# Kernel tuning notes

Hardware: AMD Instinct MI355X
Metric: run time of the kernel (lower is better)

The kernel has to match this reference:

```python
import jax, jax.numpy as jnp
import numpy as np

NUM_HEADS = 16
THETA = 10000.0
B, S, D = 2, 2048, 1024
D_K = D // NUM_HEADS


def setup_inputs() -> dict:
    key = jax.random.key(0)
    ks = jax.random.split(key, 5)
    s = 0.02
    return {
        "x": jax.random.normal(ks[0], (B, S, D), dtype=jnp.float32),
        "W_q": jax.random.normal(ks[1], (D, D), dtype=jnp.float32) * s,
        "W_k": jax.random.normal(ks[2], (D, D), dtype=jnp.float32) * s,
        "W_v": jax.random.normal(ks[3], (D, D), dtype=jnp.float32) * s,
        "W_o": jax.random.normal(ks[4], (D, D), dtype=jnp.float32) * s,
        "token_positions": jnp.arange(S, dtype=jnp.int32),
    }


def _rope(x, token_positions):
    # x: [..., seq, d_k]; equivalent to the block-diagonal 2x2 rotation matmul
    d2 = x.shape[-1] // 2
    inv_freq = THETA ** (-(2.0 * jnp.arange(d2, dtype=x.dtype)) / x.shape[-1])  # [d2]
    ang = token_positions.astype(x.dtype)[:, None] * inv_freq[None, :]  # [seq, d2]
    cos, sin = jnp.cos(ang), jnp.sin(ang)
    xp = x.reshape(x.shape[:-1] + (d2, 2))
    xe, xo = xp[..., 0], xp[..., 1]
    oe = cos * xe - sin * xo
    oo = sin * xe + cos * xo
    return jnp.stack([oe, oo], axis=-1).reshape(x.shape)


def reference(x, W_q, W_k, W_v, W_o, token_positions):
    seq = x.shape[-2]
    # QKV projections (weights stored as [out, in])
    Q = jnp.einsum('bsd,ed->bse', x, W_q)
    K = jnp.einsum('bsd,ed->bse', x, W_k)
    V = jnp.einsum('bsd,ed->bse', x, W_v)
    def split_heads(t):
        return t.reshape(t.shape[:-1] + (NUM_HEADS, D_K)).swapaxes(-3, -2)  # [b,h,s,dk]
    Q, K, V = split_heads(Q), split_heads(K), split_heads(V)
    Q = _rope(Q, token_positions)
    K = _rope(K, token_positions)
    scale = 1.0 / np.sqrt(D_K)
    scores = jnp.einsum('bhqd,bhkd->bhqk', Q, K) * scale
    causal = jnp.tril(jnp.ones((seq, seq), dtype=bool))
    scores = jnp.where(causal, scores, -jnp.inf)
    probs = jax.nn.softmax(scores, axis=-1)
    out = jnp.einsum('bhqk,bhkd->bhqd', probs, V)
    out = out.swapaxes(-3, -2).reshape(x.shape[:-1] + (D,))
    return jnp.einsum('bse,de->bsd', out, W_o)
```

## Files before the change

### kernel.cpp

```cpp
#include <hip/hip_runtime.h>
#include <hip/hip_bf16.h>
#include <math.h>

#define H_    16
#define DK_   64
#define Dm    1024
#define Bb    2
#define Ss    2048
#define Mrows 4096
#define QSCALE 0.1803368801f

typedef short s16x8 __attribute__((ext_vector_type(8)));
typedef float f32x4 __attribute__((ext_vector_type(4)));
typedef unsigned short u16;
typedef unsigned int u32;

__device__ __forceinline__ u16 f2b(float f) {
  __hip_bfloat16 h = __float2bfloat16(f);
  return *reinterpret_cast<u16*>(&h);
}
__device__ __forceinline__ float b2f(u16 u) {
  __hip_bfloat16 h;
  *reinterpret_cast<u16*>(&h) = u;
  return __bfloat162float(h);
}
__device__ __forceinline__ u32 pkbf(float hi, float lo) {
  return __builtin_amdgcn_perm(__float_as_uint(hi), __float_as_uint(lo), 0x07060302u);
}

#define GLDS(g, l)                                                             \
  __builtin_amdgcn_global_load_lds(                                            \
      (const __attribute__((address_space(1))) unsigned int*)(g),              \
      (__attribute__((address_space(3))) unsigned int*)(l), 16, 0, 0)

__device__ __forceinline__ int SW64(int row, int col) {
  return row * 64 + ((((col >> 3) ^ (row & 7) ^ (row >> 3)) & 7) << 3) + (col & 7);
}

__global__ __launch_bounds__(256) void k_castall(
    const float* __restrict__ x,  const float* __restrict__ Wq,
    const float* __restrict__ Wk, const float* __restrict__ Wv,
    const float* __restrict__ Wo,
    u16* __restrict__ xb,  u16* __restrict__ wqb, u16* __restrict__ wkb,
    u16* __restrict__ wvb, u16* __restrict__ wob,
    const int* __restrict__ pos, float2* __restrict__ tab) {
  if (blockIdx.x >= 8192) {
    int t = (blockIdx.x - 8192) * 256 + threadIdx.x;
    int s = t >> 5, i = t & 31;
    float p = (float)pos[s];
    float ang = p * powf(10000.0f, -(float)i / 32.0f);
    tab[t] = make_float2(cosf(ang), sinf(ang));
    return;
  }
  int i = blockIdx.x * 256 + threadIdx.x;
  const float* s;
  u16* d;
  int off;
  if (i < 1048576) { s = x; d = xb; off = i; }
  else {
    int j = i - 1048576;
    int w = j >> 18;
    off = j & 262143;
    s = (w == 0) ? Wq : (w == 1) ? Wk : (w == 2) ? Wv : Wo;
    d = (w == 0) ? wqb : (w == 1) ? wkb : (w == 2) ? wvb : wob;
  }
  float4 v = reinterpret_cast<const float4*>(s)[off];
  ushort4 o;
  o.x = f2b(v.x); o.y = f2b(v.y); o.z = f2b(v.z); o.w = f2b(v.w);
  reinterpret_cast<ushort4*>(d)[off] = o;
}

__global__ __launch_bounds__(256) void k_ropeK(u16* __restrict__ K,
                                               const float2* __restrict__ tab) {
  int t = blockIdx.x * 256 + threadIdx.x;
  int row = t >> 7;
  int c0 = (t & 127) << 3;
  int i0 = (c0 & 63) >> 1;
  const float2* tb = &tab[(row & (Ss - 1)) * 32 + i0];
  float2 cs[4];
#pragma unroll
  for (int j = 0; j < 4; ++j) cs[j] = tb[j];
  size_t off = (size_t)row * Dm + c0;
  s16x8 k = *reinterpret_cast<const s16x8*>(&K[off]);
  s16x8 ko;
#pragma unroll
  for (int j = 0; j < 4; ++j) {
    float ke = b2f((u16)k[2 * j]), kd = b2f((u16)k[2 * j + 1]);
    ko[2 * j]     = (short)f2b(cs[j].x * ke - cs[j].y * kd);
    ko[2 * j + 1] = (short)f2b(cs[j].y * ke + cs[j].x * kd);
  }
  *reinterpret_cast<s16x8*>(&K[off]) = ko;
}

template <int BN, bool QKV>
__global__ __launch_bounds__(256) void k_gemm(
    const u16* __restrict__ A, const u16* __restrict__ B,
    u16* __restrict__ OQ, u16* __restrict__ OK2, u16* __restrict__ OVT,
    float* __restrict__ OF, int K) {
  constexpr int NFR = BN / 32;
  __shared__ __align__(16) u16 lsA[2][128 * 32];
  __shared__ __align__(16) u16 lsB[2][BN * 32];
  const int tid = threadIdx.x, lane = tid & 63, wave = tid >> 6;
  const int quad = lane >> 4, l16 = lane & 15;
  const int wrow = wave >> 1, wcol = wave & 1;
  const int n0 = blockIdx.x * BN, m0 = blockIdx.y * 128;
  f32x4 acc[4][NFR] = {};

  auto stage = [&](int k0, int bi) {
#pragma unroll
    for (int c = 0; c < 2; ++c) {
      int f = (wave * 2 + c) * 64 + lane;
      int row = f >> 2;
      int gs = (f & 3) ^ ((row >> 1) & 3);
      GLDS(A + (size_t)(m0 + row) * K + k0 + gs * 8, &lsA[bi][(wave * 2 + c) * 512]);
    }
#pragma unroll
    for (int c = 0; c < NFR / 2; ++c) {
      int f = (wave * (NFR / 2) + c) * 64 + lane;
      int row = f >> 2;
      int gs = (f & 3) ^ ((row >> 1) & 3);
      GLDS(B + (size_t)(n0 + row) * K + k0 + gs * 8, &lsB[bi][(wave * (NFR / 2) + c) * 512]);
    }
  };

  stage(0, 0);
  int bi = 0;
  for (int k0 = 0; k0 < K; k0 += 32) {
    __syncthreads();
    if (k0 + 32 < K) stage(k0 + 32, bi ^ 1);
    s16x8 af[4], bfr[NFR];
#pragma unroll
    for (int i = 0; i < 4; ++i) {
      int row = wrow * 64 + i * 16 + l16;
      af[i] = *reinterpret_cast<const s16x8*>(
          &lsA[bi][row * 32 + ((quad ^ ((row >> 1) & 3)) << 3)]);
    }
#pragma unroll
    for (int i = 0; i < NFR; ++i) {
      int row = wcol * (BN / 2) + i * 16 + l16;
      bfr[i] = *reinterpret_cast<const s16x8*>(
          &lsB[bi][row * 32 + ((quad ^ ((row >> 1) & 3)) << 3)]);
    }
#pragma unroll
    for (int mi = 0; mi < 4; ++mi)
#pragma unroll
      for (int ni = 0; ni < NFR; ++ni)
        acc[mi][ni] = __builtin_amdgcn_mfma_f32_16x16x32_bf16(af[mi], bfr[ni], acc[mi][ni], 0, 0, 0);
    bi ^= 1;
  }

  if (QKV) {
    const int which = n0 >> 10;
    const int nbase = (n0 & 1023) + wcol * (BN / 2);
    if (which == 2) {
#pragma unroll
      for (int mi = 0; mi < 4; ++mi)
#pragma unroll
        for (int ni = 0; ni < NFR; ++ni) {
          int row0 = m0 + wrow * 64 + mi * 16 + quad * 4;
          int col  = nbase + ni * 16 + l16;
          int bb = row0 >> 11, s0 = row0 & (Ss - 1);
          ushort4 pk;
          pk.x = f2b(acc[mi][ni][0]); pk.y = f2b(acc[mi][ni][1]);
          pk.z = f2b(acc[mi][ni][2]); pk.w = f2b(acc[mi][ni][3]);
          *reinterpret_cast<ushort4*>(&OVT[((size_t)bb * Dm + col) * Ss + s0]) = pk;
        }
    } else {
      u16* Op = which ? OK2 : OQ;
#pragma unroll
      for (int mi = 0; mi < 4; ++mi)
#pragma unroll
        for (int ni = 0; ni < NFR; ++ni)
#pragma unroll
          for (int r = 0; r < 4; ++r) {
            int row = m0 + wrow * 64 + mi * 16 + quad * 4 + r;
            int col = nbase + ni * 16 + l16;
            Op[(size_t)row * Dm + col] = f2b(acc[mi][ni][r]);
          }
    }
  } else {
#pragma unroll
    for (int mi = 0; mi < 4; ++mi)
#pragma unroll
      for (int ni = 0; ni < NFR; ++ni)
#pragma unroll
        for (int r = 0; r < 4; ++r) {
          int row = m0 + wrow * 64 + mi * 16 + quad * 4 + r;
          int col = n0 + wcol * (BN / 2) + ni * 16 + l16;
          OF[(size_t)row * Dm + col] = acc[mi][ni][r];
        }
  }
}

__global__ __launch_bounds__(256) void k_flash(const u16* __restrict__ Q,
                                               const u16* __restrict__ K,
                                               const u16* __restrict__ VT,
                                               u16* __restrict__ O,
                                               const float2* __restrict__ tab) {
  __shared__ __align__(16) u16 lsK[4][64 * 64];
  __shared__ __align__(16) u16 lsVT[4][64 * 64];
  __shared__ __align__(16) u16 lsP[4][32 * 64];
  const int tid = threadIdx.x, lane = tid & 63, wave = tid >> 6;
  const int quad = lane >> 4, l16 = lane & 15;
  const int bid = blockIdx.x;
  const int bh = bid & 31;
  const int h = bh & (H_ - 1), b = bh >> 4;
  const int g = bid >> 5, a = g & 7, bsel = g >> 3;
  const int qt = bsel ? (15 - a) : a;
  const int q0 = qt * 128;
  const int qbase = q0 + wave * 32;
  const int ktmax_w = (qbase + 31) >> 6;
  const int xorv = (l16 * 2) & 0xE;

  s16x8 qf[2][2];
#pragma unroll
  for (int s = 0; s < 2; ++s) {
    const int qpos = qbase + s * 16 + l16;
    const size_t qoff = (size_t)(b * Ss + qpos) * Dm + h * 64;
    s16x8 r0 = *reinterpret_cast<const s16x8*>(&Q[qoff + quad * 8]);
    s16x8 r1 = *reinterpret_cast<const s16x8*>(&Q[qoff + 32 + quad * 8]);
    const float2* tb = &tab[(qpos & (Ss - 1)) * 32];
#pragma unroll
    for (int kc = 0; kc < 2; ++kc) {
      s16x8 raw = kc ? r1 : r0;
#pragma unroll
      for (int p = 0; p < 4; ++p) {
        float2 cs = tb[kc * 16 + quad * 4 + p];
        float e = b2f((u16)raw[2 * p]), o = b2f((u16)raw[2 * p + 1]);
        qf[s][kc][2 * p]     = (short)f2b((cs.x * e - cs.y * o) * QSCALE);
        qf[s][kc][2 * p + 1] = (short)f2b((cs.y * e + cs.x * o) * QSCALE);
      }
    }
  }
  s16x8 ones;
#pragma unroll
  for (int j = 0; j < 8; ++j) ones[j] = (short)0x3F80;

  f32x4 ot[2][4] = {};
  f32x4 lAcc[2] = {};

  auto stagepair = [&](int pp) {
#pragma unroll
    for (int half = 0; half < 2; ++half) {
      const int kt = pp * 2 + half;
      const int slot = kt & 3;
      const size_t kbase  = (size_t)(b * Ss + kt * 64) * Dm + h * 64;
      const size_t vtbase = ((size_t)b * Dm + h * 64) * Ss + kt * 64;
#pragma unroll
      for (int c = 0; c < 2; ++c) {
        int sl = (wave * 2 + c) * 64 + lane;
        int row = sl >> 3;
        int gg = ((sl & 7) ^ (row & 7) ^ (row >> 3)) & 7;
        GLDS(K  + kbase  + (size_t)row * Dm + gg * 8, &lsK[slot][(wave * 2 + c) * 512]);
        GLDS(VT + vtbase + (size_t)row * Ss + gg * 8, &lsVT[slot][(wave * 2 + c) * 512]);
      }
    }
  };

  stagepair(0);
  for (int pp = 0; pp <= qt; ++pp) {
    __syncthreads();
    if (pp < qt) stagepair(pp + 1);
    const int kt0 = 2 * pp;

    f32x4 st[2][2][4] = {};
#pragma unroll
    for (int half = 0; half < 2; ++half) {
      const int kt = kt0 + half;
      if (kt > ktmax_w) break;
      const int slot = kt & 3;
#pragma unroll
      for (int kc = 0; kc < 2; ++kc)
#pragma unroll
        for (int ni = 0; ni < 4; ++ni) {
          s16x8 kf = *reinterpret_cast<const s16x8*>(
              &lsK[slot][SW64(ni * 16 + l16, kc * 32 + quad * 8)]);
          st[half][0][ni] = __builtin_amdgcn_mfma_f32_16x16x32_bf16(kf, qf[0][kc], st[half][0][ni], 0, 0, 0);
          st[half][1][ni] = __builtin_amdgcn_mfma_f32_16x16x32_bf16(kf, qf[1][kc], st[half][1][ni], 0, 0, 0);
        }
    }
#pragma unroll
    for (int half = 0; half < 2; ++half) {
      const int kt = kt0 + half;
      if (kt > ktmax_w) break;
      const int slot = kt & 3;
      if (kt == ktmax_w) {
#pragma unroll
        for (int s = 0; s < 2; ++s) {
          int gq = qbase + s * 16 + l16;
#pragma unroll
          for (int ni = 0; ni < 4; ++ni)
#pragma unroll
            for (int r = 0; r < 4; ++r)
              if (kt * 64 + ni * 16 + quad * 4 + r > gq) st[half][s][ni][r] = -INFINITY;
        }
      }
#pragma unroll
      for (int s = 0; s < 2; ++s)
#pragma unroll
        for (int ni = 0; ni < 4; ++ni) {
          float e0 = __builtin_amdgcn_exp2f(st[half][s][ni][0]);
          float e1 = __builtin_amdgcn_exp2f(st[half][s][ni][1]);
          float e2 = __builtin_amdgcn_exp2f(st[half][s][ni][2]);
          float e3 = __builtin_amdgcn_exp2f(st[half][s][ni][3]);
          uint2 pk;
          pk.x = pkbf(e1, e0);
          pk.y = pkbf(e3, e2);
          *reinterpret_cast<uint2*>(
              &lsP[wave][(s * 16 + l16) * 64 + (((ni * 4 + quad) ^ xorv) << 2)]) = pk;
        }
#pragma unroll
      for (int kc = 0; kc < 2; ++kc) {
        s16x8 pf0 = *reinterpret_cast<const s16x8*>(
            &lsP[wave][l16 * 64 + (((kc * 8 + quad * 2) ^ xorv) << 2)]);
        s16x8 pf1 = *reinterpret_cast<const s16x8*>(
            &lsP[wave][(16 + l16) * 64 + (((kc * 8 + quad * 2) ^ xorv) << 2)]);
        lAcc[0] = __builtin_amdgcn_mfma_f32_16x16x32_bf16(ones, pf0, lAcc[0], 0, 0, 0);
        lAcc[1] = __builtin_amdgcn_mfma_f32_16x16x32_bf16(ones, pf1, lAcc[1], 0, 0, 0);
#pragma unroll
        for (int ni = 0; ni < 4; ++ni) {
          s16x8 vf = *reinterpret_cast<const s16x8*>(
              &lsVT[slot][SW64(ni * 16 + l16, kc * 32 + quad * 8)]);
          ot[0][ni] = __builtin_amdgcn_mfma_f32_16x16x32_bf16(vf, pf0, ot[0][ni], 0, 0, 0);
          ot[1][ni] = __builtin_amdgcn_mfma_f32_16x16x32_bf16(vf, pf1, ot[1][ni], 0, 0, 0);
        }
      }
    }
  }

#pragma unroll
  for (int s = 0; s < 2; ++s) {
    float inv = 1.0f / lAcc[s][0];
    const size_t obase = (size_t)(b * Ss + qbase + s * 16 + l16) * Dm + h * 64;
#pragma unroll
    for (int ni = 0; ni < 4; ++ni) {
      ushort4 pk;
      pk.x = f2b(ot[s][ni][0] * inv); pk.y = f2b(ot[s][ni][1] * inv);
      pk.z = f2b(ot[s][ni][2] * inv); pk.w = f2b(ot[s][ni][3] * inv);
      *reinterpret_cast<ushort4*>(&O[obase + ni * 16 + quad * 4]) = pk;
    }
  }
}

extern "C" void kernel_launch(void* const* d_in, const int* in_sizes, int n_in,
                              void* d_out, int out_size, void* d_ws, size_t ws_size,
                              hipStream_t stream) {
  const float* x  = (const float*)d_in[0];
  const float* Wq = (const float*)d_in[1];
  const float* Wk = (const float*)d_in[2];
  const float* Wv = (const float*)d_in[3];
  const float* Wo = (const float*)d_in[4];
  const int* pos  = (const int*)d_in[5];
  float* out = (float*)d_out;

  char* w = (char*)d_ws;
  u16* xb  = (u16*)w; w += (size_t)Mrows * Dm * 2;
  u16* wqb = (u16*)w; w += (size_t)Dm * Dm * 2;
  u16* wkb = (u16*)w; w += (size_t)Dm * Dm * 2;
  u16* wvb = (u16*)w; w += (size_t)Dm * Dm * 2;
  u16* wob = (u16*)w; w += (size_t)Dm * Dm * 2;
  u16* Qb  = (u16*)w; w += (size_t)Mrows * Dm * 2;
  u16* Kb  = (u16*)w; w += (size_t)Mrows * Dm * 2;
  u16* VTb = (u16*)w; w += (size_t)Mrows * Dm * 2;
  u16* Ab  = (u16*)w; w += (size_t)Mrows * Dm * 2;
  float2* tabf = (float2*)w; w += (size_t)Ss * 32 * sizeof(float2);

  k_castall<<<8448, 256, 0, stream>>>(x, Wq, Wk, Wv, Wo, xb, wqb, wkb, wvb, wob,
                                      pos, tabf);
  k_gemm<128, true><<<dim3(24, 32), 256, 0, stream>>>(xb, wqb, Qb, Kb, VTb, nullptr, Dm);
  k_ropeK<<<Mrows * Dm / 8 / 256, 256, 0, stream>>>(Kb, tabf);
  k_flash<<<dim3(512), 256, 0, stream>>>(Qb, Kb, VTb, Ab, tabf);
  k_gemm<64, false><<<dim3(16, 32), 256, 0, stream>>>(Ab, wob, nullptr, nullptr, nullptr, out, Dm);
}
```

Before: 186.3 us.

## Split long causal flash tiles across two blocks and combine partials

The flash attention kernel now takes its work from a 24-entry schedule table. The 8 longest query tiles (qt 8..15) are split into two KV-range halves, so each half runs in a separate block. This balances work across 768 blocks instead of 512 uneven ones. Partial outputs and row sums are written in fp32 to scratch, which reuses the output buffer and the xb workspace. A new combine kernel then sums them and normalizes. The cost is an extra launch plus extra global traffic for the fp32 partials. Because the two halves are merged by simple summation with no max rescale, the split relies on the existing un-rescaled softmax accumulation.

```diff
diff --git a/kernel.cpp b/kernel.cpp
--- a/kernel.cpp
+++ b/kernel.cpp
@@ -192,21 +192,30 @@
   }
 }
 
+__device__ const signed char T_QT[24] = {15,15,14, 7,14,13,13,12, 6,12,11,11,
+                                         10, 5,10, 9, 9, 8, 4, 8, 3, 2, 1, 0};
+__device__ const signed char T_PS[24] = { 0, 8, 0, 0, 8, 0, 7, 0, 0, 7, 0, 6,
+                                          0, 0, 6, 0, 5, 0, 0, 5, 0, 0, 0, 0};
+__device__ const signed char T_PE[24] = { 8,16, 8, 8,15, 7,14, 7, 7,13, 6,12,
+                                          6, 6,11, 5,10, 5, 5, 9, 4, 3, 2, 1};
+
 __global__ __launch_bounds__(256) void k_flash(const u16* __restrict__ Q,
                                                const u16* __restrict__ K,
                                                const u16* __restrict__ VT,
                                                u16* __restrict__ O,
-                                               const float2* __restrict__ tab) {
+                                               const float2* __restrict__ tab,
+                                               float* __restrict__ Op,
+                                               float* __restrict__ Lp) {
   __shared__ __align__(16) u16 lsK[4][64 * 64];
   __shared__ __align__(16) u16 lsVT[4][64 * 64];
   __shared__ __align__(16) u16 lsP[4][32 * 64];
   const int tid = threadIdx.x, lane = tid & 63, wave = tid >> 6;
   const int quad = lane >> 4, l16 = lane & 15;
   const int bid = blockIdx.x;
-  const int bh = bid & 31;
+  const int j = bid >> 5, bh = bid & 31;
+  const int qt = T_QT[j];
+  const int ps = T_PS[j], pe = T_PE[j];
   const int h = bh & (H_ - 1), b = bh >> 4;
-  const int g = bid >> 5, a = g & 7, bsel = g >> 3;
-  const int qt = bsel ? (15 - a) : a;
   const int q0 = qt * 128;
   const int qbase = q0 + wave * 32;
   const int ktmax_w = (qbase + 31) >> 6;
@@ -234,7 +243,7 @@
   }
   s16x8 ones;
 #pragma unroll
-  for (int j = 0; j < 8; ++j) ones[j] = (short)0x3F80;
+  for (int j2 = 0; j2 < 8; ++j2) ones[j2] = (short)0x3F80;
 
   f32x4 ot[2][4] = {};
   f32x4 lAcc[2] = {};
@@ -257,10 +266,10 @@
     }
   };
 
-  stagepair(0);
-  for (int pp = 0; pp <= qt; ++pp) {
+  stagepair(ps);
+  for (int pp = ps; pp < pe; ++pp) {
     __syncthreads();
-    if (pp < qt) stagepair(pp + 1);
+    if (pp + 1 < pe) stagepair(pp + 1);
     const int kt0 = 2 * pp;
 
     f32x4 st[2][2][4] = {};
@@ -328,18 +337,53 @@
     }
   }
 
-#pragma unroll
-  for (int s = 0; s < 2; ++s) {
-    float inv = 1.0f / lAcc[s][0];
-    const size_t obase = (size_t)(b * Ss + qbase + s * 16 + l16) * Dm + h * 64;
-#pragma unroll
-    for (int ni = 0; ni < 4; ++ni) {
-      ushort4 pk;
-      pk.x = f2b(ot[s][ni][0] * inv); pk.y = f2b(ot[s][ni][1] * inv);
-      pk.z = f2b(ot[s][ni][2] * inv); pk.w = f2b(ot[s][ni][3] * inv);
-      *reinterpret_cast<ushort4*>(&O[obase + ni * 16 + quad * 4]) = pk;
-    }
-  }
+  if (ps == 0 && pe == qt + 1) {
+#pragma unroll
+    for (int s = 0; s < 2; ++s) {
+      float inv = 1.0f / lAcc[s][0];
+      const size_t obase = (size_t)(b * Ss + qbase + s * 16 + l16) * Dm + h * 64;
+#pragma unroll
+      for (int ni = 0; ni < 4; ++ni) {
+        ushort4 pk;
+        pk.x = f2b(ot[s][ni][0] * inv); pk.y = f2b(ot[s][ni][1] * inv);
+        pk.z = f2b(ot[s][ni][2] * inv); pk.w = f2b(ot[s][ni][3] * inv);
+        *reinterpret_cast<ushort4*>(&O[obase + ni * 16 + quad * 4]) = pk;
+      }
+    }
+  } else {
+    const int part = ps ? 1 : 0;
+    const int slot = ((bh << 3) + (qt - 8)) * 2 + part;
+    float* Ob = Op + (size_t)slot * 8192;
+    float* Lb = Lp + slot * 128;
+#pragma unroll
+    for (int s = 0; s < 2; ++s) {
+      int qi = wave * 32 + s * 16 + l16;
+      if (quad == 0) Lb[qi] = lAcc[s][0];
+#pragma unroll
+      for (int ni = 0; ni < 4; ++ni)
+        *reinterpret_cast<f32x4*>(&Ob[(size_t)qi * 64 + ni * 16 + quad * 4]) = ot[s][ni];
+    }
+  }
+}
+
+__global__ __launch_bounds__(256) void k_combine(const float* __restrict__ Op,
+                                                 const float* __restrict__ Lp,
+                                                 u16* __restrict__ O) {
+  int t = blockIdx.x * 256 + threadIdx.x;
+  int dk4 = t & 15, qi = (t >> 4) & 127, tile = t >> 11;
+  int bh = tile >> 3, qt = 8 + (tile & 7);
+  int slot = tile * 2;
+  const float* O0 = Op + (size_t)slot * 8192;
+  const float* O1 = Op + (size_t)(slot + 1) * 8192;
+  float inv = 1.0f / (Lp[slot * 128 + qi] + Lp[(slot + 1) * 128 + qi]);
+  f32x4 a = *reinterpret_cast<const f32x4*>(&O0[(size_t)qi * 64 + dk4 * 4]);
+  f32x4 c = *reinterpret_cast<const f32x4*>(&O1[(size_t)qi * 64 + dk4 * 4]);
+  int b = bh >> 4, h = bh & (H_ - 1);
+  size_t obase = (size_t)(b * Ss + qt * 128 + qi) * Dm + h * 64;
+  ushort4 pk;
+  pk.x = f2b((a[0] + c[0]) * inv); pk.y = f2b((a[1] + c[1]) * inv);
+  pk.z = f2b((a[2] + c[2]) * inv); pk.w = f2b((a[3] + c[3]) * inv);
+  *reinterpret_cast<ushort4*>(&O[obase + dk4 * 4]) = pk;
 }
 
 extern "C" void kernel_launch(void* const* d_in, const int* in_sizes, int n_in,
@@ -364,11 +408,14 @@
   u16* VTb = (u16*)w; w += (size_t)Mrows * Dm * 2;
   u16* Ab  = (u16*)w; w += (size_t)Mrows * Dm * 2;
   float2* tabf = (float2*)w; w += (size_t)Ss * 32 * sizeof(float2);
+  float* op = (float*)d_out;
+  float* lp = (float*)xb;
 
   k_castall<<<8448, 256, 0, stream>>>(x, Wq, Wk, Wv, Wo, xb, wqb, wkb, wvb, wob,
                                       pos, tabf);
   k_gemm<128, true><<<dim3(24, 32), 256, 0, stream>>>(xb, wqb, Qb, Kb, VTb, nullptr, Dm);
   k_ropeK<<<Mrows * Dm / 8 / 256, 256, 0, stream>>>(Kb, tabf);
-  k_flash<<<dim3(512), 256, 0, stream>>>(Qb, Kb, VTb, Ab, tabf);
+  k_flash<<<dim3(768), 256, 0, stream>>>(Qb, Kb, VTb, Ab, tabf, op, lp);
+  k_combine<<<2048, 256, 0, stream>>>(op, lp, Ab);
   k_gemm<64, false><<<dim3(16, 32), 256, 0, stream>>>(Ab, wob, nullptr, nullptr, nullptr, out, Dm);
 }
```

Result: slower. 192.6 us (+3.4%).
